# Performance work log

Measured on AMD Instinct MI355X. Metric: run time of the kernel, lower is better.

## Reference

```python
import jax, jax.numpy as jnp
import numpy as np

N_NODES = 100000
N_EDGES = 1600000
IN_DIM, HID, OUT_DIM = 128, 128, 64


def _glorot(key, fan_in, fan_out):
    s = float(np.sqrt(6.0 / (fan_in + fan_out)))
    return jax.random.uniform(key, (fan_in, fan_out), jnp.float32, -s, s)


def setup_inputs() -> dict:
    key = jax.random.key(0)
    ks = jax.random.split(key, 6)
    x = jax.random.normal(ks[0], (N_NODES, IN_DIM), jnp.float32)
    edge_index = jax.random.randint(ks[1], (2, N_EDGES), 0, N_NODES, jnp.int32)
    return {
        "x": x,
        "edge_index": edge_index,
        "W0": _glorot(ks[2], IN_DIM, HID), "b0": jnp.zeros((HID,), jnp.float32),
        "W1": _glorot(ks[3], HID, HID),    "b1": jnp.zeros((HID,), jnp.float32),
        "W2": _glorot(ks[4], HID, OUT_DIM), "b2": jnp.zeros((OUT_DIM,), jnp.float32),
    }


def _gcn_conv(x, src, dst, norm, W, b):
    # x' = D^{-1/2} (A+I) D^{-1/2} X W + b  (PyG GCNConv, add_self_loops=True)
    h = x @ W                       # [N, F_out]
    msg = h[src] * norm[:, None]    # [E+N, F_out] gathered, normalized messages
    out = jax.ops.segment_sum(msg, dst, num_segments=x.shape[0])
    return out + b


def reference(x, edge_index, W0, b0, W1, b1, W2, b2):
    n = x.shape[0]
    loop = jnp.arange(n, dtype=edge_index.dtype)
    src = jnp.concatenate([edge_index[0], loop])  # self-loops appended
    dst = jnp.concatenate([edge_index[1], loop])
    deg = jax.ops.segment_sum(jnp.ones_like(src, jnp.float32), dst, num_segments=n)
    dis = jnp.where(deg > 0, jax.lax.rsqrt(jnp.maximum(deg, 1e-12)), 0.0)
    norm = dis[src] * dis[dst]      # symmetric GCN normalization per edge

    h = jax.nn.relu(_gcn_conv(x, src, dst, norm, W0, b0))
    h = jax.nn.relu(_gcn_conv(h, src, dst, norm, W1, b1))
    h = jax.nn.relu(_gcn_conv(h, src, dst, norm, W2, b2))
    return jax.nn.log_softmax(h, axis=1)
```

## Files before the change

### kernel.cpp

```cpp
#include <hip/hip_runtime.h>

#define NN 100000
#define NE 1600000
#define NBK 782
#define NBLK 512
#define CHUNK ((NE + NBLK - 1) / NBLK)

typedef __bf16 bf16x4 __attribute__((ext_vector_type(4)));
typedef __bf16 bf16x8 __attribute__((ext_vector_type(8)));
typedef float f32x2 __attribute__((ext_vector_type(2)));
typedef float f32x4 __attribute__((ext_vector_type(4)));

#define ACC8_FP8(vv)                                                                  \
  {                                                                                   \
    f32x2 p;                                                                          \
    p = __builtin_amdgcn_cvt_pk_f32_fp8((vv).x, 0); acc[0] += p[0]; acc[1] += p[1];   \
    p = __builtin_amdgcn_cvt_pk_f32_fp8((vv).x, 1); acc[2] += p[0]; acc[3] += p[1];   \
    p = __builtin_amdgcn_cvt_pk_f32_fp8((vv).y, 0); acc[4] += p[0]; acc[5] += p[1];   \
    p = __builtin_amdgcn_cvt_pk_f32_fp8((vv).y, 1); acc[6] += p[0]; acc[7] += p[1];   \
  }


__global__ __launch_bounds__(256) void k1_hist(const int* __restrict__ dst, int* __restrict__ bhist,
                                               const float* __restrict__ W0, const float* __restrict__ W1,
                                               const float* __restrict__ W2, __bf16* __restrict__ Wt) {
  int b = blockIdx.x;
  if (b >= NBLK) {
    int i = (b - NBLK) * 256 + threadIdx.x;
    if (i < 16384) {
      int k = i >> 7, n = i & 127;
      Wt[n * 128 + k] = (__bf16)W0[i];
    } else if (i < 32768) {
      int j = i - 16384;
      int k = j >> 7, n = j & 127;
      Wt[16384 + n * 128 + k] = (__bf16)W1[j];
    } else if (i < 40960) {
      int j = i - 32768;
      int k = j >> 6, n = j & 63;
      Wt[32768 + n * 128 + k] = (__bf16)W2[j];
    }
    return;
  }
  __shared__ int h[NBK];
  int tid = threadIdx.x;
  for (int i = tid; i < NBK; i += 256) h[i] = 0;
  __syncthreads();
  int base = b * CHUNK, end = min(base + CHUNK, NE);
  for (int e = base + tid; e < end; e += 256) atomicAdd(&h[dst[e] >> 7], 1);
  __syncthreads();
  for (int i = tid; i < NBK; i += 256) bhist[(size_t)i * NBLK + b] = h[i];
}

__global__ __launch_bounds__(256) void kA2(const int* __restrict__ bhist, int* __restrict__ btot) {
  int w = threadIdx.x >> 6, lane = threadIdx.x & 63;
  int bin = blockIdx.x * 4 + w;
  if (bin >= NBK) return;
  const int* row = bhist + (size_t)bin * NBLK + lane * 8;
  int4 v0 = *(const int4*)(row);
  int4 v1 = *(const int4*)(row + 4);
  int s = v0.x + v0.y + v0.z + v0.w + v1.x + v1.y + v1.z + v1.w;
#pragma unroll
  for (int off = 32; off > 0; off >>= 1) s += __shfl_xor(s, off);
  if (lane == 0) btot[bin] = s;
}

__global__ __launch_bounds__(1024) void kB_bscan(const int* __restrict__ btot, int* __restrict__ bptr) {
  __shared__ int ws[16];
  int tid = threadIdx.x, lane = tid & 63, w = tid >> 6;
  int v = (tid < NBK) ? btot[tid] : 0;
  int incl = v;
#pragma unroll
  for (int off = 1; off < 64; off <<= 1) {
    int t = __shfl_up(incl, off);
    if (lane >= off) incl += t;
  }
  if (lane == 63) ws[w] = incl;
  __syncthreads();
  if (tid < 16) {
    int s = ws[tid];
    int si = s;
#pragma unroll
    for (int off = 1; off < 16; off <<= 1) {
      int t = __shfl_up(si, off);
      if (lane >= off) si += t;
    }
    ws[tid] = si - s;
  }
  __syncthreads();
  if (tid < NBK) bptr[tid + 1] = incl + ws[w];
  if (tid == 0) bptr[0] = 0;
}

__global__ __launch_bounds__(256) void kC2(const int* __restrict__ bhist, const int* __restrict__ bptr,
                                           int* __restrict__ blockbase) {
  int w = threadIdx.x >> 6, lane = threadIdx.x & 63;
  int bin = blockIdx.x * 4 + w;
  if (bin >= NBK) return;
  const int* row = bhist + (size_t)bin * NBLK + lane * 8;
  int4 q0 = *(const int4*)(row);
  int4 q1 = *(const int4*)(row + 4);
  int v[8] = {q0.x, q0.y, q0.z, q0.w, q1.x, q1.y, q1.z, q1.w};
  int s = 0;
#pragma unroll
  for (int i = 0; i < 8; ++i) s += v[i];
  int incl = s;
#pragma unroll
  for (int off = 1; off < 64; off <<= 1) {
    int t = __shfl_up(incl, off);
    if (lane >= off) incl += t;
  }
  int run = bptr[bin] + incl - s;
  int* out = blockbase + (size_t)bin * NBLK + lane * 8;
  int4 o0, o1;
  o0.x = run; run += v[0];
  o0.y = run; run += v[1];
  o0.z = run; run += v[2];
  o0.w = run; run += v[3];
  o1.x = run; run += v[4];
  o1.y = run; run += v[5];
  o1.z = run; run += v[6];
  o1.w = run; run += v[7];
  *(int4*)(out) = o0;
  *(int4*)(out + 4) = o1;
}

__global__ __launch_bounds__(256) void k3_scatter(const int* __restrict__ src, const int* __restrict__ dst,
                                                  const int* __restrict__ blockbase, int* __restrict__ bucketed) {
  __shared__ int cur[NBK];
  int tid = threadIdx.x, b = blockIdx.x;
  for (int i = tid; i < NBK; i += 256) cur[i] = blockbase[(size_t)i * NBLK + b];
  __syncthreads();
  int base = b * CHUNK, end = min(base + CHUNK, NE);
  for (int e = base + tid; e < end; e += 256) {
    int d = dst[e];
    int pos = atomicAdd(&cur[d >> 7], 1);
    bucketed[pos] = (src[e] << 7) | (d & 127);
  }
}

__global__ __launch_bounds__(256) void k_degfill(const int* __restrict__ bucketed, const int* __restrict__ bptr,
                                                 int* __restrict__ row_ptr, float* __restrict__ dis,
                                                 int* __restrict__ csr_src) {
  __shared__ int deg[128];
  __shared__ int sc[128];
  __shared__ int cur[128];
  int b = blockIdx.x, tid = threadIdx.x;
  int nb0 = b << 7;
  if (tid < 128) deg[tid] = 0;
  __syncthreads();
  int beg = bptr[b], end = bptr[b + 1];
  for (int e = beg + tid; e < end; e += 256) atomicAdd(&deg[bucketed[e] & 127], 1);
  __syncthreads();
  if (tid < 128) sc[tid] = deg[tid];
  __syncthreads();
  for (int off = 1; off < 128; off <<= 1) {
    int t = (tid >= off && tid < 128) ? sc[tid - off] : 0;
    __syncthreads();
    if (tid < 128) sc[tid] += t;
    __syncthreads();
  }
  if (tid < 128) {
    cur[tid] = beg + sc[tid] - deg[tid];
    if (nb0 + tid < NN) {
      row_ptr[nb0 + tid + 1] = beg + sc[tid];
      dis[nb0 + tid] = rsqrtf((float)(deg[tid] + 1));
      if (b == 0 && tid == 0) row_ptr[0] = 0;
    }
  }
  __syncthreads();
  for (int e = beg + tid; e < end; e += 256) {
    int pk = bucketed[e];
    int pos = atomicAdd(&cur[pk & 127], 1);
    csr_src[pos] = pk >> 7;
  }
}


template <int BN, int MODE, bool OUT8>
__global__ __launch_bounds__(512) void k_gemm(const void* __restrict__ Av, const __bf16* __restrict__ Wt,
                                              const float* __restrict__ bias, const float* __restrict__ dis,
                                              void* __restrict__ outv) {
  constexpr int LDK = 136;
  constexpr int NT = BN / 32;
  constexpr int ROWB = BN * (OUT8 ? 1 : 2);
  __shared__ __bf16 lB[BN * LDK];

  const int tid = threadIdx.x;
  const int rowBase = blockIdx.x * 128;
  const int lane = tid & 63;
  const int wid = tid >> 6;
  const int wm = (wid & 3) * 32;
  const int wn = (wid >> 2) * (BN / 2);
  const int lm = lane & 15;
  const int kg = lane >> 4;

  if (blockIdx.x == 0 && tid < ROWB / 16) {
    ((uint4*)((char*)outv + (size_t)NN * ROWB))[tid] = make_uint4(0, 0, 0, 0);
  }

  for (int c = tid; c < 16 * BN; c += 512) {
    int n = c >> 4;
    int koff = (c & 15) * 8;
    *(bf16x8*)&lB[n * LDK + koff] = *(const bf16x8*)(Wt + n * 128 + koff);
  }
  __syncthreads();

  f32x4 acc[2][NT] = {};
  const bool full = (rowBase + 128 <= NN);

#pragma unroll 2
  for (int ks = 0; ks < 128; ks += 32) {
    int k0 = ks + kg * 8;
    bf16x8 af[2];
    if constexpr (MODE == 0) {
      const float* A = (const float*)Av;
#pragma unroll
      for (int tm = 0; tm < 2; ++tm) {
        int gr = rowBase + wm + tm * 16 + lm;
        f32x4 a0 = {}, a1 = {};
        if (full || gr < NN) {
          a0 = *(const f32x4*)(A + (size_t)gr * 128 + k0);
          a1 = *(const f32x4*)(A + (size_t)gr * 128 + k0 + 4);
        }
        af[tm] = bf16x8{(__bf16)a0[0], (__bf16)a0[1], (__bf16)a0[2], (__bf16)a0[3],
                        (__bf16)a1[0], (__bf16)a1[1], (__bf16)a1[2], (__bf16)a1[3]};
      }
    } else {
      const __bf16* A = (const __bf16*)Av;
      f32x4 b0 = *(const f32x4*)(bias + k0);
      f32x4 b1 = *(const f32x4*)(bias + k0 + 4);
#pragma unroll
      for (int tm = 0; tm < 2; ++tm) {
        int gr = rowBase + wm + tm * 16 + lm;
        bf16x8 v = {};
        if (full || gr < NN) v = *(const bf16x8*)(A + (size_t)gr * 128 + k0);
        af[tm] = bf16x8{(__bf16)fmaxf((float)v[0] + b0[0], 0.f), (__bf16)fmaxf((float)v[1] + b0[1], 0.f),
                        (__bf16)fmaxf((float)v[2] + b0[2], 0.f), (__bf16)fmaxf((float)v[3] + b0[3], 0.f),
                        (__bf16)fmaxf((float)v[4] + b1[0], 0.f), (__bf16)fmaxf((float)v[5] + b1[1], 0.f),
                        (__bf16)fmaxf((float)v[6] + b1[2], 0.f), (__bf16)fmaxf((float)v[7] + b1[3], 0.f)};
      }
    }
    bf16x8 bfr[NT];
#pragma unroll
    for (int tn = 0; tn < NT; ++tn)
      bfr[tn] = *(const bf16x8*)&lB[(wn + tn * 16 + lm) * LDK + k0];
#pragma unroll
    for (int tm = 0; tm < 2; ++tm)
#pragma unroll
      for (int tn = 0; tn < NT; ++tn)
        acc[tm][tn] = __builtin_amdgcn_mfma_f32_16x16x32_bf16(af[tm], bfr[tn], acc[tm][tn], 0, 0, 0);
  }

#pragma unroll
  for (int tm = 0; tm < 2; ++tm) {
    int r0 = rowBase + wm + tm * 16 + kg * 4;
#pragma unroll
    for (int tn = 0; tn < NT; ++tn) {
      int c0 = wn + tn * 16 + lm;
#pragma unroll
      for (int r = 0; r < 4; ++r) {
        int gr = r0 + r;
        if (full || gr < NN) {
          float val = acc[tm][tn][r] * dis[gr];
          if constexpr (OUT8) {
            unsigned char* o8 = (unsigned char*)outv;
            unsigned pk = __builtin_amdgcn_cvt_pk_fp8_f32(val, val, 0, 0);
            o8[(size_t)gr * BN + c0] = (unsigned char)(pk & 0xffu);
          } else {
            __bf16* ob = (__bf16*)outv;
            ob[(size_t)gr * BN + c0] = (__bf16)val;
          }
        }
      }
    }
  }
}


__global__ __launch_bounds__(256) void k_agg128(const unsigned char* __restrict__ tmp8, const int* __restrict__ row_ptr,
                                                const int* __restrict__ csr_src, const float* __restrict__ dis,
                                                __bf16* __restrict__ agg) {
  int qw = (blockIdx.x * 256 + threadIdx.x) >> 6;
  int lane = threadIdx.x & 63;
  int g = lane >> 4;
  int fl = lane & 15;
  int node = qw * 4 + g;

  int beg = row_ptr[node];
  int end = row_ptr[node + 1];

  int mx = end - beg;
  mx = max(mx, __shfl_xor(mx, 16));
  mx = max(mx, __shfl_xor(mx, 32));

  float acc[8] = {};
  {
    uint2 sv = *(const uint2*)(tmp8 + (size_t)node * 128 + fl * 8);
    ACC8_FP8(sv);
  }

  for (int done = 0; done < mx; done += 16) {
    int ep = beg + done + fl;
    int sidx = (ep < end) ? csr_src[ep] : NN;
    int rem = mx - done;
    {
      uint2 v[8];
#pragma unroll
      for (int u = 0; u < 8; ++u) {
        int s = __shfl(sidx, g * 16 + u);
        v[u] = *(const uint2*)(tmp8 + (size_t)s * 128 + fl * 8);
      }
#pragma unroll
      for (int u = 0; u < 8; ++u) ACC8_FP8(v[u]);
    }
    if (rem > 8) {
      uint2 v[8];
#pragma unroll
      for (int u = 0; u < 8; ++u) {
        int s = __shfl(sidx, g * 16 + 8 + u);
        v[u] = *(const uint2*)(tmp8 + (size_t)s * 128 + fl * 8);
      }
#pragma unroll
      for (int u = 0; u < 8; ++u) ACC8_FP8(v[u]);
    }
  }

  float d = dis[node];
  bf16x8 o;
#pragma unroll
  for (int t = 0; t < 8; ++t) o[t] = (__bf16)(acc[t] * d);
  *(bf16x8*)&agg[(size_t)node * 128 + fl * 8] = o;
}


__global__ __launch_bounds__(256) void k_agg64_final(const __bf16* __restrict__ tmp, const int* __restrict__ row_ptr,
                                                     const int* __restrict__ csr_src, const float* __restrict__ dis,
                                                     const float* __restrict__ b2, float* __restrict__ out) {
  int qw = (blockIdx.x * 256 + threadIdx.x) >> 6;
  int lane = threadIdx.x & 63;
  int g = lane >> 4;
  int fl = lane & 15;
  int node = qw * 4 + g;

  int beg = row_ptr[node];
  int end = row_ptr[node + 1];

  int mx = end - beg;
  mx = max(mx, __shfl_xor(mx, 16));
  mx = max(mx, __shfl_xor(mx, 32));

  float acc[4] = {};
  {
    bf16x4 sv = *(const bf16x4*)&tmp[(size_t)node * 64 + fl * 4];
#pragma unroll
    for (int t = 0; t < 4; ++t) acc[t] = (float)sv[t];
  }

  for (int done = 0; done < mx; done += 16) {
    int ep = beg + done + fl;
    int sidx = (ep < end) ? csr_src[ep] : NN;
    int rem = mx - done;
    {
      bf16x4 v[8];
#pragma unroll
      for (int u = 0; u < 8; ++u) {
        int s = __shfl(sidx, g * 16 + u);
        v[u] = *(const bf16x4*)&tmp[(size_t)s * 64 + fl * 4];
      }
#pragma unroll
      for (int u = 0; u < 8; ++u)
#pragma unroll
        for (int t = 0; t < 4; ++t) acc[t] += (float)v[u][t];
    }
    if (rem > 8) {
      bf16x4 v[8];
#pragma unroll
      for (int u = 0; u < 8; ++u) {
        int s = __shfl(sidx, g * 16 + 8 + u);
        v[u] = *(const bf16x4*)&tmp[(size_t)s * 64 + fl * 4];
      }
#pragma unroll
      for (int u = 0; u < 8; ++u)
#pragma unroll
        for (int t = 0; t < 4; ++t) acc[t] += (float)v[u][t];
    }
  }

  float d = dis[node];
  float v4[4], lm = -1e30f;
#pragma unroll
  for (int t = 0; t < 4; ++t) {
    v4[t] = fmaxf(acc[t] * d + b2[fl * 4 + t], 0.f);
    lm = fmaxf(lm, v4[t]);
  }
#pragma unroll
  for (int off = 8; off > 0; off >>= 1) lm = fmaxf(lm, __shfl_xor(lm, off));
  float le = 0.f;
#pragma unroll
  for (int t = 0; t < 4; ++t) le += __expf(v4[t] - lm);
#pragma unroll
  for (int off = 8; off > 0; off >>= 1) le += __shfl_xor(le, off);
  float ls = lm + __logf(le);
  f32x4 o = {v4[0] - ls, v4[1] - ls, v4[2] - ls, v4[3] - ls};
  *(f32x4*)&out[(size_t)node * 64 + fl * 4] = o;
}


extern "C" void kernel_launch(void* const* d_in, const int* in_sizes, int n_in,
                              void* d_out, int out_size, void* d_ws, size_t ws_size,
                              hipStream_t stream) {
  const float* x  = (const float*)d_in[0];
  const int*   ei = (const int*)d_in[1];
  const float* W0 = (const float*)d_in[2];
  const float* b0 = (const float*)d_in[3];
  const float* W1 = (const float*)d_in[4];
  const float* b1 = (const float*)d_in[5];
  const float* W2 = (const float*)d_in[6];
  const float* b2 = (const float*)d_in[7];
  const int* esrc = ei;
  const int* edst = ei + NE;

  char* p = (char*)d_ws;
  auto alloc = [&](size_t bytes) {
    char* q = p;
    p += (bytes + 255) & ~(size_t)255;
    return q;
  };
  float*  dis     = (float*)alloc((size_t)NN * 4);
  int*    row_ptr = (int*)alloc((size_t)(NN + 1) * 4);
  int*    btot    = (int*)alloc(NBK * 4);
  int*    bptr    = (int*)alloc((NBK + 1) * 4);
  __bf16* Wt      = (__bf16*)alloc(40960 * 2);
  int*    csr_src = (int*)alloc((size_t)NE * 4);
  char*   tmp     = (char*)alloc((size_t)(NN + 1) * 128 * 2);
  unsigned char* tmp8 = (unsigned char*)tmp;
  __bf16* tmp16   = (__bf16*)tmp;
  int*    bucketed  = (int*)tmp;
  int*    bhist     = csr_src;
  int*    blockbase = csr_src + NBK * NBLK;

  k1_hist<<<NBLK + 160, 256, 0, stream>>>(edst, bhist, W0, W1, W2, Wt);
  kA2<<<(NBK + 3) / 4, 256, 0, stream>>>(bhist, btot);
  kB_bscan<<<1, 1024, 0, stream>>>(btot, bptr);
  kC2<<<(NBK + 3) / 4, 256, 0, stream>>>(bhist, bptr, blockbase);
  k3_scatter<<<NBLK, 256, 0, stream>>>(esrc, edst, blockbase, bucketed);
  k_degfill<<<NBK, 256, 0, stream>>>(bucketed, bptr, row_ptr, dis, csr_src);

  int gblocks = (NN + 127) / 128;
  int ablocks = NN / 16;

  k_gemm<128, 0, true><<<gblocks, 512, 0, stream>>>(x, Wt, nullptr, dis, tmp8);
  k_agg128<<<ablocks, 256, 0, stream>>>(tmp8, row_ptr, csr_src, dis, (__bf16*)d_out);

  k_gemm<128, 2, true><<<gblocks, 512, 0, stream>>>(d_out, Wt + 16384, b0, dis, tmp8);
  k_agg128<<<ablocks, 256, 0, stream>>>(tmp8, row_ptr, csr_src, dis, (__bf16*)d_out);

  k_gemm<64, 2, false><<<gblocks, 512, 0, stream>>>(d_out, Wt + 32768, b1, dis, tmp16);
  k_agg64_final<<<ablocks, 256, 0, stream>>>(tmp16, row_ptr, csr_src, dis, b2, (float*)d_out);
}
```

Measured before the change: 318.0 us.

## Fuse neighbor aggregation with next-layer GEMM via shared-memory tile

Merges the fp8 aggregation kernel with the following layer's GEMM. Each 512-thread block gathers 128 node rows into LDS, then applies bias, ReLU and the MFMA matmul directly from LDS. This removes the bf16 intermediate write and re-read through global memory and two kernel launches. In exchange it uses a large LDS footprint and fewer, heavier blocks, which lowers occupancy for the latency-bound gather phase. It also adds separate ping-pong buffers.

```diff
diff --git a/kernel.cpp b/kernel.cpp
--- a/kernel.cpp
+++ b/kernel.cpp
@@ -212,33 +212,17 @@
   for (int ks = 0; ks < 128; ks += 32) {
     int k0 = ks + kg * 8;
     bf16x8 af[2];
-    if constexpr (MODE == 0) {
-      const float* A = (const float*)Av;
-#pragma unroll
-      for (int tm = 0; tm < 2; ++tm) {
-        int gr = rowBase + wm + tm * 16 + lm;
-        f32x4 a0 = {}, a1 = {};
-        if (full || gr < NN) {
-          a0 = *(const f32x4*)(A + (size_t)gr * 128 + k0);
-          a1 = *(const f32x4*)(A + (size_t)gr * 128 + k0 + 4);
-        }
-        af[tm] = bf16x8{(__bf16)a0[0], (__bf16)a0[1], (__bf16)a0[2], (__bf16)a0[3],
-                        (__bf16)a1[0], (__bf16)a1[1], (__bf16)a1[2], (__bf16)a1[3]};
-      }
-    } else {
-      const __bf16* A = (const __bf16*)Av;
-      f32x4 b0 = *(const f32x4*)(bias + k0);
-      f32x4 b1 = *(const f32x4*)(bias + k0 + 4);
-#pragma unroll
-      for (int tm = 0; tm < 2; ++tm) {
-        int gr = rowBase + wm + tm * 16 + lm;
-        bf16x8 v = {};
-        if (full || gr < NN) v = *(const bf16x8*)(A + (size_t)gr * 128 + k0);
-        af[tm] = bf16x8{(__bf16)fmaxf((float)v[0] + b0[0], 0.f), (__bf16)fmaxf((float)v[1] + b0[1], 0.f),
-                        (__bf16)fmaxf((float)v[2] + b0[2], 0.f), (__bf16)fmaxf((float)v[3] + b0[3], 0.f),
-                        (__bf16)fmaxf((float)v[4] + b1[0], 0.f), (__bf16)fmaxf((float)v[5] + b1[1], 0.f),
-                        (__bf16)fmaxf((float)v[6] + b1[2], 0.f), (__bf16)fmaxf((float)v[7] + b1[3], 0.f)};
-      }
+    const float* A = (const float*)Av;
+#pragma unroll
+    for (int tm = 0; tm < 2; ++tm) {
+      int gr = rowBase + wm + tm * 16 + lm;
+      f32x4 a0 = {}, a1 = {};
+      if (full || gr < NN) {
+        a0 = *(const f32x4*)(A + (size_t)gr * 128 + k0);
+        a1 = *(const f32x4*)(A + (size_t)gr * 128 + k0 + 4);
+      }
+      af[tm] = bf16x8{(__bf16)a0[0], (__bf16)a0[1], (__bf16)a0[2], (__bf16)a0[3],
+                      (__bf16)a1[0], (__bf16)a1[1], (__bf16)a1[2], (__bf16)a1[3]};
     }
     bf16x8 bfr[NT];
 #pragma unroll
@@ -277,59 +261,139 @@
 }
 
 
-__global__ __launch_bounds__(256) void k_agg128(const unsigned char* __restrict__ tmp8, const int* __restrict__ row_ptr,
-                                                const int* __restrict__ csr_src, const float* __restrict__ dis,
-                                                __bf16* __restrict__ agg) {
-  int qw = (blockIdx.x * 256 + threadIdx.x) >> 6;
-  int lane = threadIdx.x & 63;
-  int g = lane >> 4;
-  int fl = lane & 15;
-  int node = qw * 4 + g;
-
-  int beg = row_ptr[node];
-  int end = row_ptr[node + 1];
-
-  int mx = end - beg;
-  mx = max(mx, __shfl_xor(mx, 16));
-  mx = max(mx, __shfl_xor(mx, 32));
-
-  float acc[8] = {};
-  {
-    uint2 sv = *(const uint2*)(tmp8 + (size_t)node * 128 + fl * 8);
-    ACC8_FP8(sv);
-  }
-
-  for (int done = 0; done < mx; done += 16) {
-    int ep = beg + done + fl;
-    int sidx = (ep < end) ? csr_src[ep] : NN;
-    int rem = mx - done;
+template <int BN, bool OUT8>
+__global__ __launch_bounds__(512) void k_agg_gemm(const unsigned char* __restrict__ in8,
+                                                  const int* __restrict__ row_ptr, const int* __restrict__ csr_src,
+                                                  const float* __restrict__ dis, const __bf16* __restrict__ Wt,
+                                                  const float* __restrict__ bias, void* __restrict__ outv) {
+  constexpr int LDK = 136;
+  constexpr int NT = BN / 32;
+  constexpr int ROWB = BN * (OUT8 ? 1 : 2);
+  __shared__ __bf16 lA[128 * LDK];
+  __shared__ __bf16 lB[BN * LDK];
+
+  const int tid = threadIdx.x;
+  const int tileBase = blockIdx.x * 128;
+  const int lane = tid & 63;
+  const int wv = tid >> 6;
+  const int g = lane >> 4;
+  const int fl = lane & 15;
+
+  if (blockIdx.x == 0 && tid < ROWB / 16) {
+    ((uint4*)((char*)outv + (size_t)NN * ROWB))[tid] = make_uint4(0, 0, 0, 0);
+  }
+
+  for (int c = tid; c < 16 * BN; c += 512) {
+    int n = c >> 4;
+    int koff = (c & 15) * 8;
+    *(bf16x8*)&lB[n * LDK + koff] = *(const bf16x8*)(Wt + n * 128 + koff);
+  }
+
+  for (int it = 0; it < 4; ++it) {
+    int lrow = it * 32 + wv * 4 + g;
+    int node = tileBase + lrow;
+    int beg = 0, end = 0;
+    if (node < NN) { beg = row_ptr[node]; end = row_ptr[node + 1]; }
+    int nd = (node < NN) ? node : NN;
+
+    int mx = end - beg;
+    mx = max(mx, __shfl_xor(mx, 16));
+    mx = max(mx, __shfl_xor(mx, 32));
+
+    float acc[8] = {};
     {
-      uint2 v[8];
-#pragma unroll
-      for (int u = 0; u < 8; ++u) {
-        int s = __shfl(sidx, g * 16 + u);
-        v[u] = *(const uint2*)(tmp8 + (size_t)s * 128 + fl * 8);
-      }
-#pragma unroll
-      for (int u = 0; u < 8; ++u) ACC8_FP8(v[u]);
-    }
-    if (rem > 8) {
-      uint2 v[8];
-#pragma unroll
-      for (int u = 0; u < 8; ++u) {
-        int s = __shfl(sidx, g * 16 + 8 + u);
-        v[u] = *(const uint2*)(tmp8 + (size_t)s * 128 + fl * 8);
-      }
-#pragma unroll
-      for (int u = 0; u < 8; ++u) ACC8_FP8(v[u]);
-    }
-  }
-
-  float d = dis[node];
-  bf16x8 o;
-#pragma unroll
-  for (int t = 0; t < 8; ++t) o[t] = (__bf16)(acc[t] * d);
-  *(bf16x8*)&agg[(size_t)node * 128 + fl * 8] = o;
+      uint2 sv = *(const uint2*)(in8 + (size_t)nd * 128 + fl * 8);
+      ACC8_FP8(sv);
+    }
+    for (int done = 0; done < mx; done += 16) {
+      int ep = beg + done + fl;
+      int sidx = (ep < end) ? csr_src[ep] : NN;
+      int rem = mx - done;
+      {
+        uint2 v[8];
+#pragma unroll
+        for (int u = 0; u < 8; ++u) {
+          int s = __shfl(sidx, g * 16 + u);
+          v[u] = *(const uint2*)(in8 + (size_t)s * 128 + fl * 8);
+        }
+#pragma unroll
+        for (int u = 0; u < 8; ++u) ACC8_FP8(v[u]);
+      }
+      if (rem > 8) {
+        uint2 v[8];
+#pragma unroll
+        for (int u = 0; u < 8; ++u) {
+          int s = __shfl(sidx, g * 16 + 8 + u);
+          v[u] = *(const uint2*)(in8 + (size_t)s * 128 + fl * 8);
+        }
+#pragma unroll
+        for (int u = 0; u < 8; ++u) ACC8_FP8(v[u]);
+      }
+    }
+    float d = (node < NN) ? dis[node] : 0.f;
+    bf16x8 o;
+#pragma unroll
+    for (int t = 0; t < 8; ++t) o[t] = (__bf16)(acc[t] * d);
+    *(bf16x8*)&lA[lrow * LDK + fl * 8] = o;
+  }
+  __syncthreads();
+
+  const int wm = (wv & 3) * 32;
+  const int wn = (wv >> 2) * (BN / 2);
+  const int lm = lane & 15;
+  const int kg = lane >> 4;
+  const bool full = (tileBase + 128 <= NN);
+
+  f32x4 acc2[2][NT] = {};
+#pragma unroll 2
+  for (int ks = 0; ks < 128; ks += 32) {
+    int k0 = ks + kg * 8;
+    f32x4 b0 = *(const f32x4*)(bias + k0);
+    f32x4 b1 = *(const f32x4*)(bias + k0 + 4);
+    bf16x8 af[2];
+#pragma unroll
+    for (int tm = 0; tm < 2; ++tm) {
+      int lr = wm + tm * 16 + lm;
+      bf16x8 v = *(const bf16x8*)&lA[lr * LDK + k0];
+      af[tm] = bf16x8{(__bf16)fmaxf((float)v[0] + b0[0], 0.f), (__bf16)fmaxf((float)v[1] + b0[1], 0.f),
+                      (__bf16)fmaxf((float)v[2] + b0[2], 0.f), (__bf16)fmaxf((float)v[3] + b0[3], 0.f),
+                      (__bf16)fmaxf((float)v[4] + b1[0], 0.f), (__bf16)fmaxf((float)v[5] + b1[1], 0.f),
+                      (__bf16)fmaxf((float)v[6] + b1[2], 0.f), (__bf16)fmaxf((float)v[7] + b1[3], 0.f)};
+    }
+    bf16x8 bfr[NT];
+#pragma unroll
+    for (int tn = 0; tn < NT; ++tn)
+      bfr[tn] = *(const bf16x8*)&lB[(wn + tn * 16 + lm) * LDK + k0];
+#pragma unroll
+    for (int tm = 0; tm < 2; ++tm)
+#pragma unroll
+      for (int tn = 0; tn < NT; ++tn)
+        acc2[tm][tn] = __builtin_amdgcn_mfma_f32_16x16x32_bf16(af[tm], bfr[tn], acc2[tm][tn], 0, 0, 0);
+  }
+
+#pragma unroll
+  for (int tm = 0; tm < 2; ++tm) {
+    int r0 = tileBase + wm + tm * 16 + kg * 4;
+#pragma unroll
+    for (int tn = 0; tn < NT; ++tn) {
+      int c0 = wn + tn * 16 + lm;
+#pragma unroll
+      for (int r = 0; r < 4; ++r) {
+        int gr = r0 + r;
+        if (full || gr < NN) {
+          float val = acc2[tm][tn][r] * dis[gr];
+          if constexpr (OUT8) {
+            unsigned char* o8 = (unsigned char*)outv;
+            unsigned pk = __builtin_amdgcn_cvt_pk_fp8_f32(val, val, 0, 0);
+            o8[(size_t)gr * BN + c0] = (unsigned char)(pk & 0xffu);
+          } else {
+            __bf16* ob = (__bf16*)outv;
+            ob[(size_t)gr * BN + c0] = (__bf16)val;
+          }
+        }
+      }
+    }
+  }
 }
 
 
@@ -432,9 +496,12 @@
   int*    bptr    = (int*)alloc((NBK + 1) * 4);
   __bf16* Wt      = (__bf16*)alloc(40960 * 2);
   int*    csr_src = (int*)alloc((size_t)NE * 4);
-  char*   tmp     = (char*)alloc((size_t)(NN + 1) * 128 * 2);
-  unsigned char* tmp8 = (unsigned char*)tmp;
-  __bf16* tmp16   = (__bf16*)tmp;
+  char*   tmp     = (char*)alloc((size_t)(NN + 1) * 128);
+  char*   tmp_b   = (char*)alloc((size_t)(NN + 1) * 128);
+  char*   tmp_c   = (char*)alloc((size_t)(NN + 1) * 128);
+  unsigned char* tmp8   = (unsigned char*)tmp;
+  unsigned char* tmp8_b = (unsigned char*)tmp_b;
+  __bf16* tmp16_c = (__bf16*)tmp_c;
   int*    bucketed  = (int*)tmp;
   int*    bhist     = csr_src;
   int*    blockbase = csr_src + NBK * NBLK;
@@ -450,11 +517,7 @@
   int ablocks = NN / 16;
 
   k_gemm<128, 0, true><<<gblocks, 512, 0, stream>>>(x, Wt, nullptr, dis, tmp8);
-  k_agg128<<<ablocks, 256, 0, stream>>>(tmp8, row_ptr, csr_src, dis, (__bf16*)d_out);
-
-  k_gemm<128, 2, true><<<gblocks, 512, 0, stream>>>(d_out, Wt + 16384, b0, dis, tmp8);
-  k_agg128<<<ablocks, 256, 0, stream>>>(tmp8, row_ptr, csr_src, dis, (__bf16*)d_out);
-
-  k_gemm<64, 2, false><<<gblocks, 512, 0, stream>>>(d_out, Wt + 32768, b1, dis, tmp16);
-  k_agg64_final<<<ablocks, 256, 0, stream>>>(tmp16, row_ptr, csr_src, dis, b2, (float*)d_out);
-}
+  k_agg_gemm<128, true><<<gblocks, 512, 0, stream>>>(tmp8, row_ptr, csr_src, dis, Wt + 16384, b0, tmp8_b);
+  k_agg_gemm<64, false><<<gblocks, 512, 0, stream>>>(tmp8_b, row_ptr, csr_src, dis, Wt + 32768, b1, tmp16_c);
+  k_agg64_final<<<ablocks, 256, 0, stream>>>(tmp16_c, row_ptr, csr_src, dis, b2, (float*)d_out);
+}
```

Result: faster. 311.1 us (-2.2%).
